# Performance work log

Measured on AMD Instinct MI355X. Metric: run time of the kernel, lower is better.

## Reference

```python
import jax, jax.numpy as jnp
import numpy as np

N, D_IN, D_H, D_OUT, R, E, NB = 50000, 128, 128, 64, 4, 400000, 2

def _xavier(k, shape, fan_in, fan_out):
    # torch xavier_uniform with relu gain sqrt(2)
    lim = np.sqrt(2.0) * np.sqrt(6.0 / (fan_in + fan_out))
    return jax.random.uniform(k, shape, jnp.float32, -lim, lim)

def setup_inputs() -> dict:
    key = jax.random.key(0)
    ks = jax.random.split(key, 9)
    x = jax.random.normal(ks[0], (N, D_IN), dtype=jnp.float32)
    src = jax.random.randint(ks[1], (R, E), 0, N, dtype=jnp.int32)
    dst = jax.random.randint(ks[2], (R, E), 0, N, dtype=jnp.int32)
    inp = {"x": x, "src": src, "dst": dst}
    dims = [(D_IN, D_H), (D_H, D_H), (D_H, D_OUT)]
    for i, (di, do) in enumerate(dims):
        inp[f"basis{i}"] = _xavier(ks[3 + 2 * i], (NB, di, do), di, do)
        inp[f"coeff{i}"] = _xavier(ks[4 + 2 * i], (R, NB), NB, R)
    return inp

def _rel_layer(h, src, dst, basis, coeff):
    """One RelGraphConvLayer: per-relation basis weight + GraphConv(norm='both'),
    summed over relations (HeteroGraphConv aggregate='sum')."""
    n = h.shape[0]
    W = jnp.einsum('rb,bio->rio', coeff, basis)  # [R, d_in, d_out] basis-decomposed weights
    out = jnp.zeros((n, W.shape[-1]), dtype=h.dtype)
    for r in range(src.shape[0]):  # fixed small set of relations
        s, d = src[r], dst[r]
        ones = jnp.ones(s.shape[0], dtype=h.dtype)
        deg_out = jnp.maximum(jax.ops.segment_sum(ones, s, num_segments=n), 1.0)
        deg_in = jnp.maximum(jax.ops.segment_sum(ones, d, num_segments=n), 1.0)
        norm_src = deg_out ** -0.5
        norm_dst = deg_in ** -0.5
        # weight applied before aggregation (d_in >= d_out path of dgl GraphConv; math identical)
        hr = (h * norm_src[:, None]) @ W[r]            # [N, d_out]
        agg = jax.ops.segment_sum(hr[s], d, num_segments=n)  # SpMM via gather + scatter-add
        out = out + agg * norm_dst[:, None]
    return out

def reference(x, src, dst, basis0, coeff0, basis1, coeff1, basis2, coeff2):
    h = jax.nn.relu(_rel_layer(x, src, dst, basis0, coeff0))
    h = jax.nn.relu(_rel_layer(h, src, dst, basis1, coeff1))
    return _rel_layer(h, src, dst, basis2, coeff2)  # final layer: no activation
```

## Files before the change

kernel.cpp:

```cpp
#include <hip/hip_runtime.h>
#include <hip/hip_bf16.h>
#include <cstdint>
#include <cstddef>

#define NN 50000
#define RR 4
#define EE 400000
#define TE (RR*EE)
#define HR 25000
#define RN (RR*NN)
#define NSEG (NN*RR)
#define SCB2 782
#define NBK 512
#define BKSZ 98
#define CHA 4000
#define MAXSPAN 4608

using frag_ab = __attribute__((ext_vector_type(8))) short;
using frag_cd = __attribute__((ext_vector_type(4))) float;

static __device__ __forceinline__ unsigned short f2bf(float f) {
    union { float f; unsigned u; } v; v.f = f;
    unsigned r = (v.u + 0x7FFF + ((v.u >> 16) & 1)) >> 16;
    return (unsigned short)r;
}
static __device__ __forceinline__ unsigned pack2(float lo, float hi) {
    return (unsigned)f2bf(lo) | ((unsigned)f2bf(hi) << 16);
}
static __device__ __forceinline__ float blo(unsigned u) { return __uint_as_float(u << 16); }
static __device__ __forceinline__ float bhi(unsigned u) { return __uint_as_float(u & 0xFFFF0000u); }

__global__ __launch_bounds__(1024) void k_hist(const int* __restrict__ src,
                                               const int* __restrict__ dst,
                                               int* __restrict__ cnt_srcQ,
                                               int* __restrict__ cnt_dstQ) {
    __shared__ unsigned bins[HR / 2];
    int combo = blockIdx.x >> 3;
    int range = (blockIdx.x >> 2) & 1;
    int qc    = blockIdx.x & 3;
    int r = combo >> 1;
    int side = combo & 1;
    const int* arr = (side == 0 ? src : dst) + (size_t)r * EE + (size_t)qc * (EE / 4);
    int lo = range * HR;
    for (int i = threadIdx.x; i < HR / 2; i += 1024) bins[i] = 0;
    __syncthreads();
    const int4* a4 = (const int4*)arr;
    for (int i = threadIdx.x; i < EE / 16; i += 1024) {
        int4 v = a4[i];
        int t;
        t = v.x - lo; if ((unsigned)t < (unsigned)HR) atomicAdd(&bins[t >> 1], 1u << ((t & 1) * 16));
        t = v.y - lo; if ((unsigned)t < (unsigned)HR) atomicAdd(&bins[t >> 1], 1u << ((t & 1) * 16));
        t = v.z - lo; if ((unsigned)t < (unsigned)HR) atomicAdd(&bins[t >> 1], 1u << ((t & 1) * 16));
        t = v.w - lo; if ((unsigned)t < (unsigned)HR) atomicAdd(&bins[t >> 1], 1u << ((t & 1) * 16));
    }
    __syncthreads();
    int* outp = (side == 0 ? cnt_srcQ : cnt_dstQ) + (size_t)qc * RN + (size_t)r * NN + lo;
    for (int i = threadIdx.x; i < HR / 2; i += 1024) {
        unsigned b = bins[i];
        outp[2 * i]     = (int)(b & 0xFFFFu);
        outp[2 * i + 1] = (int)(b >> 16);
    }
}

__global__ __launch_bounds__(256) void k_sum_norms(const int* __restrict__ cnt_srcQ,
                                                   const int* __restrict__ cnt_dstQ,
                                                   float* __restrict__ nsrc,
                                                   float* __restrict__ ndst,
                                                   int* __restrict__ cntd2) {
    int i = blockIdx.x * 256 + threadIdx.x;
    if (i >= RN) return;
    int ss = cnt_srcQ[i] + cnt_srcQ[RN + i] + cnt_srcQ[2 * RN + i] + cnt_srcQ[3 * RN + i];
    int ds = cnt_dstQ[i] + cnt_dstQ[RN + i] + cnt_dstQ[2 * RN + i] + cnt_dstQ[3 * RN + i];
    nsrc[i] = 1.0f / sqrtf(fmaxf((float)ss, 1.0f));
    ndst[i] = 1.0f / sqrtf(fmaxf((float)ds, 1.0f));
    int r = i / NN, d = i - r * NN;
    cntd2[d * 4 + r] = ds;
}

__global__ __launch_bounds__(256) void k_partial(const int* __restrict__ cntd2,
                                                 int* __restrict__ part) {
    __shared__ int s[256];
    int t = threadIdx.x;
    int f = blockIdx.x * 256 + t;
    int v = (f < NSEG) ? cntd2[f] : 0;
    s[t] = v;
    __syncthreads();
    for (int off = 128; off > 0; off >>= 1) {
        if (t < off) s[t] += s[t + off];
        __syncthreads();
    }
    if (t == 0) part[blockIdx.x] = s[0];
}

__global__ __launch_bounds__(1024) void k_scan_small(const int* __restrict__ part,
                                                     int* __restrict__ offs) {
    __shared__ int s[1024];
    int t = threadIdx.x;
    s[t] = (t < SCB2) ? part[t] : 0;
    __syncthreads();
    for (int off = 1; off < 1024; off <<= 1) {
        int v = (t >= off) ? s[t - off] : 0;
        __syncthreads();
        s[t] += v;
        __syncthreads();
    }
    if (t < SCB2) offs[t] = (t == 0) ? 0 : s[t - 1];
}

__global__ __launch_bounds__(256) void k_emit(const int* __restrict__ cntd2,
                                              const int* __restrict__ offs,
                                              int* __restrict__ rp2) {
    __shared__ int s[256];
    int t = threadIdx.x;
    int f = blockIdx.x * 256 + t;
    int v = (f < NSEG) ? cntd2[f] : 0;
    s[t] = v;
    __syncthreads();
    for (int off = 1; off < 256; off <<= 1) {
        int u = (t >= off) ? s[t - off] : 0;
        __syncthreads();
        s[t] += u;
        __syncthreads();
    }
    if (f < NSEG) rp2[f] = offs[blockIdx.x] + s[t] - v;
    if (f == NSEG - 1) rp2[NSEG] = TE;
}

__global__ __launch_bounds__(256) void k_initg(const int* __restrict__ rp2,
                                               int* __restrict__ gcur) {
    int i = blockIdx.x * 256 + threadIdx.x;
    if (i < NBK) gcur[i] = rp2[min(i * BKSZ * 4, NSEG)];
}

__global__ __launch_bounds__(256) void k_fillA(const int* __restrict__ src,
                                               const int* __restrict__ dst,
                                               int* __restrict__ gcur,
                                               unsigned* __restrict__ stage) {
    __shared__ int cnt[NBK];
    __shared__ int rcur[NBK];
    int r = blockIdx.y;
    int base_e = blockIdx.x * CHA;
    int t = threadIdx.x;
    for (int i = t; i < NBK; i += 256) cnt[i] = 0;
    __syncthreads();
    const int* dr = dst + (size_t)r * EE;
    const int* sr = src + (size_t)r * EE;
    for (int i = base_e + t; i < base_e + CHA; i += 256) {
        int d = dr[i];
        atomicAdd(&cnt[d / BKSZ], 1);
    }
    __syncthreads();
    for (int i = t; i < NBK; i += 256) rcur[i] = atomicAdd(&gcur[i], cnt[i]);
    __syncthreads();
    for (int i = base_e + t; i < base_e + CHA; i += 256) {
        int d = dr[i];
        int s = sr[i];
        int b = d / BKSZ;
        int dl = d - b * BKSZ;
        int pos = atomicAdd(&rcur[b], 1);
        stage[pos] = (unsigned)s | ((unsigned)r << 16) | ((unsigned)dl << 18);
    }
}

__global__ __launch_bounds__(256) void k_fillB(const unsigned* __restrict__ stage,
                                               const int* __restrict__ rp2,
                                               const float* __restrict__ nsrc,
                                               const float* __restrict__ ndst,
                                               uint2* __restrict__ ed) {
    __shared__ unsigned imgU[MAXSPAN];
    __shared__ float imgW[MAXSPAN];
    __shared__ int lcur[BKSZ * 4];
    __shared__ float ndL[BKSZ * 4];
    int b = blockIdx.x;
    int t = threadIdx.x;
    int node0 = b * BKSZ;
    if (node0 >= NN) return;
    int nodes = min(BKSZ, NN - node0);
    int nseg_local = nodes * 4;
    int segbase = node0 * 4;
    for (int i = t; i < nseg_local; i += 256) {
        lcur[i] = rp2[segbase + i];
        ndL[i] = ndst[(i & 3) * NN + node0 + (i >> 2)];
    }
    __syncthreads();
    int S0 = rp2[segbase];
    int S1 = rp2[segbase + nseg_local];
    int span = S1 - S0;
    if (span <= MAXSPAN) {
        for (int i = S0 + t; i < S1; i += 256) {
            unsigned w = stage[i];
            int s = (int)(w & 0xFFFFu);
            int r = (int)((w >> 16) & 3u);
            int dl = (int)(w >> 18);
            int seg = dl * 4 + r;
            int pos = atomicAdd(&lcur[seg], 1);
            int idx = pos - S0;
            imgU[idx] = w & 0x3FFFFu;
            imgW[idx] = nsrc[r * NN + s] * ndL[seg];
        }
        __syncthreads();
        for (int i = t; i < span; i += 256)
            ed[S0 + i] = make_uint2(imgU[i], __float_as_uint(imgW[i]));
    } else {
        for (int i = S0 + t; i < S1; i += 256) {
            unsigned w = stage[i];
            int s = (int)(w & 0xFFFFu);
            int r = (int)((w >> 16) & 3u);
            int dl = (int)(w >> 18);
            int seg = dl * 4 + r;
            int pos = atomicAdd(&lcur[seg], 1);
            ed[pos] = make_uint2(w & 0x3FFFFu,
                                 __float_as_uint(nsrc[r * NN + s] * ndL[seg]));
        }
    }
}

__global__ __launch_bounds__(256) void k_cvt_x(const float4* __restrict__ x4,
                                               uint2* __restrict__ o, int n4) {
    int i = blockIdx.x * 256 + threadIdx.x;
    if (i >= n4) return;
    float4 v = x4[i];
    o[i] = make_uint2(pack2(v.x, v.y), pack2(v.z, v.w));
}

__global__ __launch_bounds__(256) void k_cvt_bt_all(const float* __restrict__ B0,
                                                    const float* __restrict__ B1,
                                                    const float* __restrict__ B2,
                                                    unsigned short* __restrict__ Bt0,
                                                    unsigned short* __restrict__ Bt1,
                                                    unsigned short* __restrict__ Bt2) {
    int o = blockIdx.x * 256 + threadIdx.x;
    if (o < 32768) {
        int k = o & 255, n = o >> 8;
        Bt0[o] = f2bf(B0[k * 128 + n]);
    } else if (o < 65536) {
        int i = o - 32768;
        int k = i & 255, n = i >> 8;
        Bt1[i] = f2bf(B1[k * 128 + n]);
    } else if (o < 81920) {
        int i = o - 65536;
        int k = i & 255, n = i >> 8;
        Bt2[i] = f2bf(B2[k * 64 + n]);
    }
}

__global__ __launch_bounds__(256) void k_agg(const uint4* __restrict__ hb4,
                                             const int* __restrict__ rp2,
                                             const uint2* __restrict__ ed,
                                             const float* __restrict__ coeff,
                                             uint2* __restrict__ Mb2) {
    int wave = (blockIdx.x * 256 + threadIdx.x) >> 6;
    int lane = threadIdx.x & 63;
    if (wave >= NN) return;
    int q = lane >> 4, hl = lane & 15;

    float c00 = coeff[0], c01 = coeff[1], c10 = coeff[2], c11 = coeff[3];
    float c20 = coeff[4], c21 = coeff[5], c30 = coeff[6], c31 = coeff[7];

    float a00 = 0.f, a01 = 0.f, a02 = 0.f, a03 = 0.f;
    float a04 = 0.f, a05 = 0.f, a06 = 0.f, a07 = 0.f;
    float a10 = 0.f, a11 = 0.f, a12 = 0.f, a13 = 0.f;
    float a14 = 0.f, a15 = 0.f, a16 = 0.f, a17 = 0.f;

    int e0 = rp2[wave * 4], e1 = rp2[wave * 4 + 4];

    int e = e0;
    uint2 wA = make_uint2(0u, 0u), wB = make_uint2(0u, 0u);
    if (e + 7 < e1) { wA = ed[e + q]; wB = ed[e + 4 + q]; }
    for (; e + 7 < e1; e += 8) {
        uint4 hA = hb4[(size_t)(wA.x & 0xFFFFu) * 16 + hl];
        uint4 hB = hb4[(size_t)(wB.x & 0xFFFFu) * 16 + hl];
        int eN = (e + 15 < e1) ? (e + 8) : e0;
        uint2 nA = ed[eN + q];
        uint2 nB = ed[eN + 4 + q];

        int rA = (int)(wA.x >> 16);
        int rB = (int)(wB.x >> 16);
        float wsA = __uint_as_float(wA.y);
        float wsB = __uint_as_float(wB.y);
        float wa0 = (rA == 0 ? c00 : rA == 1 ? c10 : rA == 2 ? c20 : c30) * wsA;
        float wa1 = (rA == 0 ? c01 : rA == 1 ? c11 : rA == 2 ? c21 : c31) * wsA;
        float wb0 = (rB == 0 ? c00 : rB == 1 ? c10 : rB == 2 ? c20 : c30) * wsB;
        float wb1 = (rB == 0 ? c01 : rB == 1 ? c11 : rB == 2 ? c21 : c31) * wsB;

        float h0 = blo(hA.x), h1 = bhi(hA.x), h2 = blo(hA.y), h3 = bhi(hA.y);
        float h4 = blo(hA.z), h5 = bhi(hA.z), h6 = blo(hA.w), h7 = bhi(hA.w);
        a00 += wa0 * h0; a01 += wa0 * h1; a02 += wa0 * h2; a03 += wa0 * h3;
        a04 += wa0 * h4; a05 += wa0 * h5; a06 += wa0 * h6; a07 += wa0 * h7;
        a10 += wa1 * h0; a11 += wa1 * h1; a12 += wa1 * h2; a13 += wa1 * h3;
        a14 += wa1 * h4; a15 += wa1 * h5; a16 += wa1 * h6; a17 += wa1 * h7;

        h0 = blo(hB.x); h1 = bhi(hB.x); h2 = blo(hB.y); h3 = bhi(hB.y);
        h4 = blo(hB.z); h5 = bhi(hB.z); h6 = blo(hB.w); h7 = bhi(hB.w);
        a00 += wb0 * h0; a01 += wb0 * h1; a02 += wb0 * h2; a03 += wb0 * h3;
        a04 += wb0 * h4; a05 += wb0 * h5; a06 += wb0 * h6; a07 += wb0 * h7;
        a10 += wb1 * h0; a11 += wb1 * h1; a12 += wb1 * h2; a13 += wb1 * h3;
        a14 += wb1 * h4; a15 += wb1 * h5; a16 += wb1 * h6; a17 += wb1 * h7;

        wA = nA; wB = nB;
    }
    for (; e < e1; e += 4) {
        int E = e + q;
        bool act = E < e1;
        uint2 weA = ed[act ? E : e0];
        uint4 hA = hb4[(size_t)(weA.x & 0xFFFFu) * 16 + hl];
        int rA = (int)(weA.x >> 16);
        float wsA = act ? __uint_as_float(weA.y) : 0.f;
        float wa0 = (rA == 0 ? c00 : rA == 1 ? c10 : rA == 2 ? c20 : c30) * wsA;
        float wa1 = (rA == 0 ? c01 : rA == 1 ? c11 : rA == 2 ? c21 : c31) * wsA;
        float h0 = blo(hA.x), h1 = bhi(hA.x), h2 = blo(hA.y), h3 = bhi(hA.y);
        float h4 = blo(hA.z), h5 = bhi(hA.z), h6 = blo(hA.w), h7 = bhi(hA.w);
        a00 += wa0 * h0; a01 += wa0 * h1; a02 += wa0 * h2; a03 += wa0 * h3;
        a04 += wa0 * h4; a05 += wa0 * h5; a06 += wa0 * h6; a07 += wa0 * h7;
        a10 += wa1 * h0; a11 += wa1 * h1; a12 += wa1 * h2; a13 += wa1 * h3;
        a14 += wa1 * h4; a15 += wa1 * h5; a16 += wa1 * h6; a17 += wa1 * h7;
    }

    a00 += __shfl_xor(a00, 16, 64); a00 += __shfl_xor(a00, 32, 64);
    a01 += __shfl_xor(a01, 16, 64); a01 += __shfl_xor(a01, 32, 64);
    a02 += __shfl_xor(a02, 16, 64); a02 += __shfl_xor(a02, 32, 64);
    a03 += __shfl_xor(a03, 16, 64); a03 += __shfl_xor(a03, 32, 64);
    a04 += __shfl_xor(a04, 16, 64); a04 += __shfl_xor(a04, 32, 64);
    a05 += __shfl_xor(a05, 16, 64); a05 += __shfl_xor(a05, 32, 64);
    a06 += __shfl_xor(a06, 16, 64); a06 += __shfl_xor(a06, 32, 64);
    a07 += __shfl_xor(a07, 16, 64); a07 += __shfl_xor(a07, 32, 64);
    a10 += __shfl_xor(a10, 16, 64); a10 += __shfl_xor(a10, 32, 64);
    a11 += __shfl_xor(a11, 16, 64); a11 += __shfl_xor(a11, 32, 64);
    a12 += __shfl_xor(a12, 16, 64); a12 += __shfl_xor(a12, 32, 64);
    a13 += __shfl_xor(a13, 16, 64); a13 += __shfl_xor(a13, 32, 64);
    a14 += __shfl_xor(a14, 16, 64); a14 += __shfl_xor(a14, 32, 64);
    a15 += __shfl_xor(a15, 16, 64); a15 += __shfl_xor(a15, 32, 64);
    a16 += __shfl_xor(a16, 16, 64); a16 += __shfl_xor(a16, 32, 64);
    a17 += __shfl_xor(a17, 16, 64); a17 += __shfl_xor(a17, 32, 64);

    int c = q >> 1, h4 = q & 1;
    float v0 = c ? (h4 ? a14 : a10) : (h4 ? a04 : a00);
    float v1 = c ? (h4 ? a15 : a11) : (h4 ? a05 : a01);
    float v2 = c ? (h4 ? a16 : a12) : (h4 ? a06 : a02);
    float v3 = c ? (h4 ? a17 : a13) : (h4 ? a07 : a03);
    uint2 st;
    st.x = pack2(v0, v1);
    st.y = pack2(v2, v3);
    Mb2[(size_t)wave * 64 + c * 32 + hl * 2 + h4] = st;
}

template <int BN, bool BF16OUT>
__global__ __launch_bounds__(256) void k_gemm(const unsigned short* __restrict__ A,
                                              const unsigned short* __restrict__ Bt,
                                              void* __restrict__ Cout) {
    int wave = threadIdx.x >> 6, lane = threadIdx.x & 63;
    int row0 = blockIdx.x * 64 + wave * 16;
    if (row0 >= NN) return;
    int m = lane & 15, q = lane >> 4;
    const int NT = BN / 16;

    frag_cd acc[NT];
#pragma unroll
    for (int ct = 0; ct < NT; ct++) acc[ct] = (frag_cd){0.f, 0.f, 0.f, 0.f};

    const size_t abase = (size_t)(row0 + m) * 256 + q * 8;
#pragma unroll
    for (int kc = 0; kc < 8; kc++) {
        frag_ab a = *(const frag_ab*)(A + abase + kc * 32);
#pragma unroll
        for (int ct = 0; ct < NT; ct++) {
            frag_ab b = *(const frag_ab*)(Bt + (size_t)(ct * 16 + m) * 256 + kc * 32 + q * 8);
            acc[ct] = __builtin_amdgcn_mfma_f32_16x16x32_bf16(a, b, acc[ct], 0, 0, 0);
        }
    }

#pragma unroll
    for (int ct = 0; ct < NT; ct++) {
#pragma unroll
        for (int i = 0; i < 4; i++) {
            int row = row0 + q * 4 + i;
            int col = ct * 16 + m;
            float v = acc[ct][i];
            if (BF16OUT) {
                v = fmaxf(v, 0.f);
                ((unsigned short*)Cout)[(size_t)row * BN + col] = f2bf(v);
            } else {
                ((float*)Cout)[(size_t)row * BN + col] = v;
            }
        }
    }
}


extern "C" void kernel_launch(void* const* d_in, const int* in_sizes, int n_in,
                              void* d_out, int out_size, void* d_ws, size_t ws_size,
                              hipStream_t stream) {
    const float* x      = (const float*)d_in[0];
    const int*   src    = (const int*)d_in[1];
    const int*   dst    = (const int*)d_in[2];
    const float* basis0 = (const float*)d_in[3];
    const float* coeff0 = (const float*)d_in[4];
    const float* basis1 = (const float*)d_in[5];
    const float* coeff1 = (const float*)d_in[6];
    const float* basis2 = (const float*)d_in[7];
    const float* coeff2 = (const float*)d_in[8];
    float* out = (float*)d_out;

    char* p = (char*)d_ws;
    auto alloc = [&](size_t bytes) {
        char* r = p;
        p += (bytes + 255) & ~(size_t)255;
        return r;
    };
    int*   cnt_srcQ = (int*)alloc((size_t)4 * RN * 4);
    int*   cnt_dstQ = (int*)alloc((size_t)4 * RN * 4);
    float* nsrc     = (float*)alloc((size_t)RN * 4);
    float* ndst     = (float*)alloc((size_t)RN * 4);
    int*   cntd2    = (int*)alloc((size_t)NSEG * 4);
    int*   rp2      = (int*)alloc((size_t)(NSEG + 1) * 4);
    int*   part     = (int*)alloc((size_t)SCB2 * 4);
    int*   offs     = (int*)alloc((size_t)SCB2 * 4);
    int*   gcur     = (int*)alloc((size_t)NBK * 4);
    unsigned* stage = (unsigned*)alloc((size_t)TE * 4);
    uint2* ed       = (uint2*)alloc((size_t)TE * 8);
    unsigned* Mb   = (unsigned*)alloc((size_t)NN * 128 * 4);
    unsigned* Hb   = (unsigned*)alloc((size_t)NN * 64 * 4);
    unsigned* Xb   = (unsigned*)alloc((size_t)NN * 64 * 4);
    unsigned short* Bt0 = (unsigned short*)alloc((size_t)128 * 256 * 2);
    unsigned short* Bt1 = (unsigned short*)alloc((size_t)128 * 256 * 2);
    unsigned short* Bt2 = (unsigned short*)alloc((size_t)64 * 256 * 2);

    k_cvt_x<<<(NN * 32 + 255) / 256, 256, 0, stream>>>((const float4*)x, (uint2*)Xb, NN * 32);
    k_cvt_bt_all<<<320, 256, 0, stream>>>(basis0, basis1, basis2, Bt0, Bt1, Bt2);
    k_hist<<<64, 1024, 0, stream>>>(src, dst, cnt_srcQ, cnt_dstQ);
    k_sum_norms<<<(RN + 255) / 256, 256, 0, stream>>>(cnt_srcQ, cnt_dstQ, nsrc, ndst, cntd2);
    k_partial<<<SCB2, 256, 0, stream>>>(cntd2, part);
    k_scan_small<<<1, 1024, 0, stream>>>(part, offs);
    k_emit<<<SCB2, 256, 0, stream>>>(cntd2, offs, rp2);
    k_initg<<<(NBK + 255) / 256, 256, 0, stream>>>(rp2, gcur);
    k_fillA<<<dim3(EE / CHA, RR), 256, 0, stream>>>(src, dst, gcur, stage);
    k_fillB<<<NBK, 256, 0, stream>>>(stage, rp2, nsrc, ndst, ed);

    int aggBlocks = NN / 4;
    int gemmBlocks = (NN + 63) / 64;

    k_agg<<<aggBlocks, 256, 0, stream>>>((const uint4*)Xb, rp2, ed, coeff0, (uint2*)Mb);
    k_gemm<128, true><<<gemmBlocks, 256, 0, stream>>>((const unsigned short*)Mb, Bt0, Hb);
    k_agg<<<aggBlocks, 256, 0, stream>>>((const uint4*)Hb, rp2, ed, coeff1, (uint2*)Mb);
    k_gemm<128, true><<<gemmBlocks, 256, 0, stream>>>((const unsigned short*)Mb, Bt1, Hb);
    k_agg<<<aggBlocks, 256, 0, stream>>>((const uint4*)Hb, rp2, ed, coeff2, (uint2*)Mb);
    k_gemm<64, false><<<gemmBlocks, 256, 0, stream>>>((const unsigned short*)Mb, Bt2, out);
}
```

Baseline: 407.9 us.

## Assign each quarter-wave one relation segment and factor coefficients out of aggregation

Each 16-lane quarter of the wave now walks the edge segment of a single relation (using per-relation row pointers rp2[wave*4+q]), accumulating 8 plain weighted sums. The basis coefficients are applied once after the loop instead of being selected and multiplied per edge. This cuts the per-edge FMAs in half and removes the relation-select logic. The cost is load imbalance across quarters when relation degrees differ, and a less coalesced edge-index load pattern with shorter unrolled chunks.

Result: slower. 418.2 us (+2.5%).

```diff
diff --git a/kernel.cpp b/kernel.cpp
--- a/kernel.cpp
+++ b/kernel.cpp
@@ -254,67 +254,52 @@
     if (wave >= NN) return;
     int q = lane >> 4, hl = lane & 15;
 
-    float c00 = coeff[0], c01 = coeff[1], c10 = coeff[2], c11 = coeff[3];
-    float c20 = coeff[4], c21 = coeff[5], c30 = coeff[6], c31 = coeff[7];
-
-    float a00 = 0.f, a01 = 0.f, a02 = 0.f, a03 = 0.f;
-    float a04 = 0.f, a05 = 0.f, a06 = 0.f, a07 = 0.f;
-    float a10 = 0.f, a11 = 0.f, a12 = 0.f, a13 = 0.f;
-    float a14 = 0.f, a15 = 0.f, a16 = 0.f, a17 = 0.f;
-
-    int e0 = rp2[wave * 4], e1 = rp2[wave * 4 + 4];
-
-    int e = e0;
+    float cq0 = coeff[2 * q];
+    float cq1 = coeff[2 * q + 1];
+
+    float s0 = 0.f, s1 = 0.f, s2 = 0.f, s3 = 0.f;
+    float s4 = 0.f, s5 = 0.f, s6 = 0.f, s7 = 0.f;
+
+    int e  = rp2[wave * 4 + q];
+    int e1 = rp2[wave * 4 + q + 1];
+
     uint2 wA = make_uint2(0u, 0u), wB = make_uint2(0u, 0u);
-    if (e + 7 < e1) { wA = ed[e + q]; wB = ed[e + 4 + q]; }
-    for (; e + 7 < e1; e += 8) {
+    if (e + 1 < e1) { wA = ed[e]; wB = ed[e + 1]; }
+    for (; e + 1 < e1; e += 2) {
         uint4 hA = hb4[(size_t)(wA.x & 0xFFFFu) * 16 + hl];
         uint4 hB = hb4[(size_t)(wB.x & 0xFFFFu) * 16 + hl];
-        int eN = (e + 15 < e1) ? (e + 8) : e0;
-        uint2 nA = ed[eN + q];
-        uint2 nB = ed[eN + 4 + q];
-
-        int rA = (int)(wA.x >> 16);
-        int rB = (int)(wB.x >> 16);
+        int eN = (e + 3 < e1) ? (e + 2) : e;
+        uint2 nA = ed[eN];
+        uint2 nB = ed[eN + 1];
         float wsA = __uint_as_float(wA.y);
         float wsB = __uint_as_float(wB.y);
-        float wa0 = (rA == 0 ? c00 : rA == 1 ? c10 : rA == 2 ? c20 : c30) * wsA;
-        float wa1 = (rA == 0 ? c01 : rA == 1 ? c11 : rA == 2 ? c21 : c31) * wsA;
-        float wb0 = (rB == 0 ? c00 : rB == 1 ? c10 : rB == 2 ? c20 : c30) * wsB;
-        float wb1 = (rB == 0 ? c01 : rB == 1 ? c11 : rB == 2 ? c21 : c31) * wsB;
-
-        float h0 = blo(hA.x), h1 = bhi(hA.x), h2 = blo(hA.y), h3 = bhi(hA.y);
-        float h4 = blo(hA.z), h5 = bhi(hA.z), h6 = blo(hA.w), h7 = bhi(hA.w);
-        a00 += wa0 * h0; a01 += wa0 * h1; a02 += wa0 * h2; a03 += wa0 * h3;
-        a04 += wa0 * h4; a05 += wa0 * h5; a06 += wa0 * h6; a07 += wa0 * h7;
-        a10 += wa1 * h0; a11 += wa1 * h1; a12 += wa1 * h2; a13 += wa1 * h3;
-        a14 += wa1 * h4; a15 += wa1 * h5; a16 += wa1 * h6; a17 += wa1 * h7;
-
-        h0 = blo(hB.x); h1 = bhi(hB.x); h2 = blo(hB.y); h3 = bhi(hB.y);
-        h4 = blo(hB.z); h5 = bhi(hB.z); h6 = blo(hB.w); h7 = bhi(hB.w);
-        a00 += wb0 * h0; a01 += wb0 * h1; a02 += wb0 * h2; a03 += wb0 * h3;
-        a04 += wb0 * h4; a05 += wb0 * h5; a06 += wb0 * h6; a07 += wb0 * h7;
-        a10 += wb1 * h0; a11 += wb1 * h1; a12 += wb1 * h2; a13 += wb1 * h3;
-        a14 += wb1 * h4; a15 += wb1 * h5; a16 += wb1 * h6; a17 += wb1 * h7;
+
+        s0 += wsA * blo(hA.x); s1 += wsA * bhi(hA.x);
+        s2 += wsA * blo(hA.y); s3 += wsA * bhi(hA.y);
+        s4 += wsA * blo(hA.z); s5 += wsA * bhi(hA.z);
+        s6 += wsA * blo(hA.w); s7 += wsA * bhi(hA.w);
+
+        s0 += wsB * blo(hB.x); s1 += wsB * bhi(hB.x);
+        s2 += wsB * blo(hB.y); s3 += wsB * bhi(hB.y);
+        s4 += wsB * blo(hB.z); s5 += wsB * bhi(hB.z);
+        s6 += wsB * blo(hB.w); s7 += wsB * bhi(hB.w);
 
         wA = nA; wB = nB;
     }
-    for (; e < e1; e += 4) {
-        int E = e + q;
-        bool act = E < e1;
-        uint2 weA = ed[act ? E : e0];
-        uint4 hA = hb4[(size_t)(weA.x & 0xFFFFu) * 16 + hl];
-        int rA = (int)(weA.x >> 16);
-        float wsA = act ? __uint_as_float(weA.y) : 0.f;
-        float wa0 = (rA == 0 ? c00 : rA == 1 ? c10 : rA == 2 ? c20 : c30) * wsA;
-        float wa1 = (rA == 0 ? c01 : rA == 1 ? c11 : rA == 2 ? c21 : c31) * wsA;
-        float h0 = blo(hA.x), h1 = bhi(hA.x), h2 = blo(hA.y), h3 = bhi(hA.y);
-        float h4 = blo(hA.z), h5 = bhi(hA.z), h6 = blo(hA.w), h7 = bhi(hA.w);
-        a00 += wa0 * h0; a01 += wa0 * h1; a02 += wa0 * h2; a03 += wa0 * h3;
-        a04 += wa0 * h4; a05 += wa0 * h5; a06 += wa0 * h6; a07 += wa0 * h7;
-        a10 += wa1 * h0; a11 += wa1 * h1; a12 += wa1 * h2; a13 += wa1 * h3;
-        a14 += wa1 * h4; a15 += wa1 * h5; a16 += wa1 * h6; a17 += wa1 * h7;
-    }
+    if (e < e1) {
+        uint2 w1 = ed[e];
+        uint4 h1 = hb4[(size_t)(w1.x & 0xFFFFu) * 16 + hl];
+        float ws = __uint_as_float(w1.y);
+        s0 += ws * blo(h1.x); s1 += ws * bhi(h1.x);
+        s2 += ws * blo(h1.y); s3 += ws * bhi(h1.y);
+        s4 += ws * blo(h1.z); s5 += ws * bhi(h1.z);
+        s6 += ws * blo(h1.w); s7 += ws * bhi(h1.w);
+    }
+
+    float a00 = cq0 * s0, a01 = cq0 * s1, a02 = cq0 * s2, a03 = cq0 * s3;
+    float a04 = cq0 * s4, a05 = cq0 * s5, a06 = cq0 * s6, a07 = cq0 * s7;
+    float a10 = cq1 * s0, a11 = cq1 * s1, a12 = cq1 * s2, a13 = cq1 * s3;
+    float a14 = cq1 * s4, a15 = cq1 * s5, a16 = cq1 * s6, a17 = cq1 * s7;
 
     a00 += __shfl_xor(a00, 16, 64); a00 += __shfl_xor(a00, 32, 64);
     a01 += __shfl_xor(a01, 16, 64); a01 += __shfl_xor(a01, 32, 64);
```

## Fuse aggregation with basis GEMM per block via swizzled LDS tile

Applied to the files above, without the earlier changes.

Merges each layer's gather-aggregate kernel and the following MFMA GEMM into one kernel. Each 512-thread block aggregates 32 nodes into a swizzled LDS tile, then runs the bf16 MFMA from LDS, so the intermediate Mb matrix no longer goes through global memory. Also merges the x and basis conversion kernels, and folds k_initg into k_emit to cut launches. The cost is lower per-block parallelism in the GEMM phase and a block-wide barrier between the gather and the matmul, plus a ping-pong buffer for layer outputs.

After: 378.3 us. 7.3% less time.

```diff
diff --git a/kernel.cpp b/kernel.cpp
--- a/kernel.cpp
+++ b/kernel.cpp
@@ -109,7 +109,8 @@
 
 __global__ __launch_bounds__(256) void k_emit(const int* __restrict__ cntd2,
                                               const int* __restrict__ offs,
-                                              int* __restrict__ rp2) {
+                                              int* __restrict__ rp2,
+                                              int* __restrict__ gcur) {
     __shared__ int s[256];
     int t = threadIdx.x;
     int f = blockIdx.x * 256 + t;
@@ -122,14 +123,15 @@
         s[t] += u;
         __syncthreads();
     }
-    if (f < NSEG) rp2[f] = offs[blockIdx.x] + s[t] - v;
-    if (f == NSEG - 1) rp2[NSEG] = TE;
-}
-
-__global__ __launch_bounds__(256) void k_initg(const int* __restrict__ rp2,
-                                               int* __restrict__ gcur) {
-    int i = blockIdx.x * 256 + threadIdx.x;
-    if (i < NBK) gcur[i] = rp2[min(i * BKSZ * 4, NSEG)];
+    if (f < NSEG) {
+        int rv = offs[blockIdx.x] + s[t] - v;
+        rp2[f] = rv;
+        if (f % (BKSZ * 4) == 0) gcur[f / (BKSZ * 4)] = rv;
+    }
+    if (f == NSEG - 1) {
+        rp2[NSEG] = TE;
+        gcur[NBK - 1] = TE;
+    }
 }
 
 __global__ __launch_bounds__(256) void k_fillA(const int* __restrict__ src,
@@ -215,172 +217,186 @@
     }
 }
 
-__global__ __launch_bounds__(256) void k_cvt_x(const float4* __restrict__ x4,
-                                               uint2* __restrict__ o, int n4) {
-    int i = blockIdx.x * 256 + threadIdx.x;
-    if (i >= n4) return;
-    float4 v = x4[i];
-    o[i] = make_uint2(pack2(v.x, v.y), pack2(v.z, v.w));
-}
-
-__global__ __launch_bounds__(256) void k_cvt_bt_all(const float* __restrict__ B0,
-                                                    const float* __restrict__ B1,
-                                                    const float* __restrict__ B2,
-                                                    unsigned short* __restrict__ Bt0,
-                                                    unsigned short* __restrict__ Bt1,
-                                                    unsigned short* __restrict__ Bt2) {
-    int o = blockIdx.x * 256 + threadIdx.x;
-    if (o < 32768) {
-        int k = o & 255, n = o >> 8;
-        Bt0[o] = f2bf(B0[k * 128 + n]);
-    } else if (o < 65536) {
-        int i = o - 32768;
-        int k = i & 255, n = i >> 8;
-        Bt1[i] = f2bf(B1[k * 128 + n]);
-    } else if (o < 81920) {
-        int i = o - 65536;
-        int k = i & 255, n = i >> 8;
-        Bt2[i] = f2bf(B2[k * 64 + n]);
-    }
-}
-
-__global__ __launch_bounds__(256) void k_agg(const uint4* __restrict__ hb4,
-                                             const int* __restrict__ rp2,
-                                             const uint2* __restrict__ ed,
-                                             const float* __restrict__ coeff,
-                                             uint2* __restrict__ Mb2) {
-    int wave = (blockIdx.x * 256 + threadIdx.x) >> 6;
+__global__ __launch_bounds__(256) void k_cvt_all(const float4* __restrict__ x4,
+                                                 uint2* __restrict__ o,
+                                                 const float* __restrict__ B0,
+                                                 const float* __restrict__ B1,
+                                                 const float* __restrict__ B2,
+                                                 unsigned short* __restrict__ Bt0,
+                                                 unsigned short* __restrict__ Bt1,
+                                                 unsigned short* __restrict__ Bt2) {
+    int b = blockIdx.x;
+    if (b < 6250) {
+        int i = b * 256 + threadIdx.x;
+        float4 v = x4[i];
+        o[i] = make_uint2(pack2(v.x, v.y), pack2(v.z, v.w));
+    } else {
+        int t = (b - 6250) * 256 + threadIdx.x;
+        if (t < 32768) {
+            int k = t & 255, n = t >> 8;
+            Bt0[t] = f2bf(B0[k * 128 + n]);
+        } else if (t < 65536) {
+            int i = t - 32768;
+            int k = i & 255, n = i >> 8;
+            Bt1[i] = f2bf(B1[k * 128 + n]);
+        } else if (t < 81920) {
+            int i = t - 65536;
+            int k = i & 255, n = i >> 8;
+            Bt2[i] = f2bf(B2[k * 64 + n]);
+        }
+    }
+}
+
+template <int BN, bool BF16OUT>
+__global__ __launch_bounds__(512) void k_agg_gemm(const uint4* __restrict__ hb4,
+                                                  const int* __restrict__ rp2,
+                                                  const uint2* __restrict__ ed,
+                                                  const float* __restrict__ coeff,
+                                                  const unsigned short* __restrict__ Bt,
+                                                  void* __restrict__ Cout) {
+    __shared__ uint4 ldsA4[32 * 32];
+    char* ldsB = (char*)ldsA4;
+
+    int w = threadIdx.x >> 6;
     int lane = threadIdx.x & 63;
-    if (wave >= NN) return;
     int q = lane >> 4, hl = lane & 15;
+    int node0 = blockIdx.x * 32;
 
     float c00 = coeff[0], c01 = coeff[1], c10 = coeff[2], c11 = coeff[3];
     float c20 = coeff[4], c21 = coeff[5], c30 = coeff[6], c31 = coeff[7];
 
-    float a00 = 0.f, a01 = 0.f, a02 = 0.f, a03 = 0.f;
-    float a04 = 0.f, a05 = 0.f, a06 = 0.f, a07 = 0.f;
-    float a10 = 0.f, a11 = 0.f, a12 = 0.f, a13 = 0.f;
-    float a14 = 0.f, a15 = 0.f, a16 = 0.f, a17 = 0.f;
-
-    int e0 = rp2[wave * 4], e1 = rp2[wave * 4 + 4];
-
-    int e = e0;
-    uint2 wA = make_uint2(0u, 0u), wB = make_uint2(0u, 0u);
-    if (e + 7 < e1) { wA = ed[e + q]; wB = ed[e + 4 + q]; }
-    for (; e + 7 < e1; e += 8) {
-        uint4 hA = hb4[(size_t)(wA.x & 0xFFFFu) * 16 + hl];
-        uint4 hB = hb4[(size_t)(wB.x & 0xFFFFu) * 16 + hl];
-        int eN = (e + 15 < e1) ? (e + 8) : e0;
-        uint2 nA = ed[eN + q];
-        uint2 nB = ed[eN + 4 + q];
-
-        int rA = (int)(wA.x >> 16);
-        int rB = (int)(wB.x >> 16);
-        float wsA = __uint_as_float(wA.y);
-        float wsB = __uint_as_float(wB.y);
-        float wa0 = (rA == 0 ? c00 : rA == 1 ? c10 : rA == 2 ? c20 : c30) * wsA;
-        float wa1 = (rA == 0 ? c01 : rA == 1 ? c11 : rA == 2 ? c21 : c31) * wsA;
-        float wb0 = (rB == 0 ? c00 : rB == 1 ? c10 : rB == 2 ? c20 : c30) * wsB;
-        float wb1 = (rB == 0 ? c01 : rB == 1 ? c11 : rB == 2 ? c21 : c31) * wsB;
-
-        float h0 = blo(hA.x), h1 = bhi(hA.x), h2 = blo(hA.y), h3 = bhi(hA.y);
-        float h4 = blo(hA.z), h5 = bhi(hA.z), h6 = blo(hA.w), h7 = bhi(hA.w);
-        a00 += wa0 * h0; a01 += wa0 * h1; a02 += wa0 * h2; a03 += wa0 * h3;
-        a04 += wa0 * h4; a05 += wa0 * h5; a06 += wa0 * h6; a07 += wa0 * h7;
-        a10 += wa1 * h0; a11 += wa1 * h1; a12 += wa1 * h2; a13 += wa1 * h3;
-        a14 += wa1 * h4; a15 += wa1 * h5; a16 += wa1 * h6; a17 += wa1 * h7;
-
-        h0 = blo(hB.x); h1 = bhi(hB.x); h2 = blo(hB.y); h3 = bhi(hB.y);
-        h4 = blo(hB.z); h5 = bhi(hB.z); h6 = blo(hB.w); h7 = bhi(hB.w);
-        a00 += wb0 * h0; a01 += wb0 * h1; a02 += wb0 * h2; a03 += wb0 * h3;
-        a04 += wb0 * h4; a05 += wb0 * h5; a06 += wb0 * h6; a07 += wb0 * h7;
-        a10 += wb1 * h0; a11 += wb1 * h1; a12 += wb1 * h2; a13 += wb1 * h3;
-        a14 += wb1 * h4; a15 += wb1 * h5; a16 += wb1 * h6; a17 += wb1 * h7;
-
-        wA = nA; wB = nB;
-    }
-    for (; e < e1; e += 4) {
-        int E = e + q;
-        bool act = E < e1;
-        uint2 weA = ed[act ? E : e0];
-        uint4 hA = hb4[(size_t)(weA.x & 0xFFFFu) * 16 + hl];
-        int rA = (int)(weA.x >> 16);
-        float wsA = act ? __uint_as_float(weA.y) : 0.f;
-        float wa0 = (rA == 0 ? c00 : rA == 1 ? c10 : rA == 2 ? c20 : c30) * wsA;
-        float wa1 = (rA == 0 ? c01 : rA == 1 ? c11 : rA == 2 ? c21 : c31) * wsA;
-        float h0 = blo(hA.x), h1 = bhi(hA.x), h2 = blo(hA.y), h3 = bhi(hA.y);
-        float h4 = blo(hA.z), h5 = bhi(hA.z), h6 = blo(hA.w), h7 = bhi(hA.w);
-        a00 += wa0 * h0; a01 += wa0 * h1; a02 += wa0 * h2; a03 += wa0 * h3;
-        a04 += wa0 * h4; a05 += wa0 * h5; a06 += wa0 * h6; a07 += wa0 * h7;
-        a10 += wa1 * h0; a11 += wa1 * h1; a12 += wa1 * h2; a13 += wa1 * h3;
-        a14 += wa1 * h4; a15 += wa1 * h5; a16 += wa1 * h6; a17 += wa1 * h7;
-    }
-
-    a00 += __shfl_xor(a00, 16, 64); a00 += __shfl_xor(a00, 32, 64);
-    a01 += __shfl_xor(a01, 16, 64); a01 += __shfl_xor(a01, 32, 64);
-    a02 += __shfl_xor(a02, 16, 64); a02 += __shfl_xor(a02, 32, 64);
-    a03 += __shfl_xor(a03, 16, 64); a03 += __shfl_xor(a03, 32, 64);
-    a04 += __shfl_xor(a04, 16, 64); a04 += __shfl_xor(a04, 32, 64);
-    a05 += __shfl_xor(a05, 16, 64); a05 += __shfl_xor(a05, 32, 64);
-    a06 += __shfl_xor(a06, 16, 64); a06 += __shfl_xor(a06, 32, 64);
-    a07 += __shfl_xor(a07, 16, 64); a07 += __shfl_xor(a07, 32, 64);
-    a10 += __shfl_xor(a10, 16, 64); a10 += __shfl_xor(a10, 32, 64);
-    a11 += __shfl_xor(a11, 16, 64); a11 += __shfl_xor(a11, 32, 64);
-    a12 += __shfl_xor(a12, 16, 64); a12 += __shfl_xor(a12, 32, 64);
-    a13 += __shfl_xor(a13, 16, 64); a13 += __shfl_xor(a13, 32, 64);
-    a14 += __shfl_xor(a14, 16, 64); a14 += __shfl_xor(a14, 32, 64);
-    a15 += __shfl_xor(a15, 16, 64); a15 += __shfl_xor(a15, 32, 64);
-    a16 += __shfl_xor(a16, 16, 64); a16 += __shfl_xor(a16, 32, 64);
-    a17 += __shfl_xor(a17, 16, 64); a17 += __shfl_xor(a17, 32, 64);
-
-    int c = q >> 1, h4 = q & 1;
-    float v0 = c ? (h4 ? a14 : a10) : (h4 ? a04 : a00);
-    float v1 = c ? (h4 ? a15 : a11) : (h4 ? a05 : a01);
-    float v2 = c ? (h4 ? a16 : a12) : (h4 ? a06 : a02);
-    float v3 = c ? (h4 ? a17 : a13) : (h4 ? a07 : a03);
-    uint2 st;
-    st.x = pack2(v0, v1);
-    st.y = pack2(v2, v3);
-    Mb2[(size_t)wave * 64 + c * 32 + hl * 2 + h4] = st;
-}
-
-template <int BN, bool BF16OUT>
-__global__ __launch_bounds__(256) void k_gemm(const unsigned short* __restrict__ A,
-                                              const unsigned short* __restrict__ Bt,
-                                              void* __restrict__ Cout) {
-    int wave = threadIdx.x >> 6, lane = threadIdx.x & 63;
-    int row0 = blockIdx.x * 64 + wave * 16;
-    if (row0 >= NN) return;
-    int m = lane & 15, q = lane >> 4;
-    const int NT = BN / 16;
-
-    frag_cd acc[NT];
+#pragma unroll 1
+    for (int k4 = 0; k4 < 4; k4++) {
+        int rowl = w + k4 * 8;
+        int node = node0 + rowl;
+        if (node < NN) {
+            float a00 = 0.f, a01 = 0.f, a02 = 0.f, a03 = 0.f;
+            float a04 = 0.f, a05 = 0.f, a06 = 0.f, a07 = 0.f;
+            float a10 = 0.f, a11 = 0.f, a12 = 0.f, a13 = 0.f;
+            float a14 = 0.f, a15 = 0.f, a16 = 0.f, a17 = 0.f;
+
+            int e0 = rp2[node * 4], e1 = rp2[node * 4 + 4];
+            int e = e0;
+            uint2 wA = make_uint2(0u, 0u), wB = make_uint2(0u, 0u);
+            if (e + 7 < e1) { wA = ed[e + q]; wB = ed[e + 4 + q]; }
+            for (; e + 7 < e1; e += 8) {
+                uint4 hA = hb4[(size_t)(wA.x & 0xFFFFu) * 16 + hl];
+                uint4 hB = hb4[(size_t)(wB.x & 0xFFFFu) * 16 + hl];
+                int eN = (e + 15 < e1) ? (e + 8) : e0;
+                uint2 nA = ed[eN + q];
+                uint2 nB = ed[eN + 4 + q];
+
+                int rA = (int)(wA.x >> 16);
+                int rB = (int)(wB.x >> 16);
+                float wsA = __uint_as_float(wA.y);
+                float wsB = __uint_as_float(wB.y);
+                float wa0 = (rA == 0 ? c00 : rA == 1 ? c10 : rA == 2 ? c20 : c30) * wsA;
+                float wa1 = (rA == 0 ? c01 : rA == 1 ? c11 : rA == 2 ? c21 : c31) * wsA;
+                float wb0 = (rB == 0 ? c00 : rB == 1 ? c10 : rB == 2 ? c20 : c30) * wsB;
+                float wb1 = (rB == 0 ? c01 : rB == 1 ? c11 : rB == 2 ? c21 : c31) * wsB;
+
+                float h0 = blo(hA.x), h1 = bhi(hA.x), h2 = blo(hA.y), h3 = bhi(hA.y);
+                float h4 = blo(hA.z), h5 = bhi(hA.z), h6 = blo(hA.w), h7 = bhi(hA.w);
+                a00 += wa0 * h0; a01 += wa0 * h1; a02 += wa0 * h2; a03 += wa0 * h3;
+                a04 += wa0 * h4; a05 += wa0 * h5; a06 += wa0 * h6; a07 += wa0 * h7;
+                a10 += wa1 * h0; a11 += wa1 * h1; a12 += wa1 * h2; a13 += wa1 * h3;
+                a14 += wa1 * h4; a15 += wa1 * h5; a16 += wa1 * h6; a17 += wa1 * h7;
+
+                h0 = blo(hB.x); h1 = bhi(hB.x); h2 = blo(hB.y); h3 = bhi(hB.y);
+                h4 = blo(hB.z); h5 = bhi(hB.z); h6 = blo(hB.w); h7 = bhi(hB.w);
+                a00 += wb0 * h0; a01 += wb0 * h1; a02 += wb0 * h2; a03 += wb0 * h3;
+                a04 += wb0 * h4; a05 += wb0 * h5; a06 += wb0 * h6; a07 += wb0 * h7;
+                a10 += wb1 * h0; a11 += wb1 * h1; a12 += wb1 * h2; a13 += wb1 * h3;
+                a14 += wb1 * h4; a15 += wb1 * h5; a16 += wb1 * h6; a17 += wb1 * h7;
+
+                wA = nA; wB = nB;
+            }
+            for (; e < e1; e += 4) {
+                int E = e + q;
+                bool act = E < e1;
+                uint2 weA = ed[act ? E : e0];
+                uint4 hA = hb4[(size_t)(weA.x & 0xFFFFu) * 16 + hl];
+                int rA = (int)(weA.x >> 16);
+                float wsA = act ? __uint_as_float(weA.y) : 0.f;
+                float wa0 = (rA == 0 ? c00 : rA == 1 ? c10 : rA == 2 ? c20 : c30) * wsA;
+                float wa1 = (rA == 0 ? c01 : rA == 1 ? c11 : rA == 2 ? c21 : c31) * wsA;
+                float h0 = blo(hA.x), h1 = bhi(hA.x), h2 = blo(hA.y), h3 = bhi(hA.y);
+                float h4 = blo(hA.z), h5 = bhi(hA.z), h6 = blo(hA.w), h7 = bhi(hA.w);
+                a00 += wa0 * h0; a01 += wa0 * h1; a02 += wa0 * h2; a03 += wa0 * h3;
+                a04 += wa0 * h4; a05 += wa0 * h5; a06 += wa0 * h6; a07 += wa0 * h7;
+                a10 += wa1 * h0; a11 += wa1 * h1; a12 += wa1 * h2; a13 += wa1 * h3;
+                a14 += wa1 * h4; a15 += wa1 * h5; a16 += wa1 * h6; a17 += wa1 * h7;
+            }
+
+            a00 += __shfl_xor(a00, 16, 64); a00 += __shfl_xor(a00, 32, 64);
+            a01 += __shfl_xor(a01, 16, 64); a01 += __shfl_xor(a01, 32, 64);
+            a02 += __shfl_xor(a02, 16, 64); a02 += __shfl_xor(a02, 32, 64);
+            a03 += __shfl_xor(a03, 16, 64); a03 += __shfl_xor(a03, 32, 64);
+            a04 += __shfl_xor(a04, 16, 64); a04 += __shfl_xor(a04, 32, 64);
+            a05 += __shfl_xor(a05, 16, 64); a05 += __shfl_xor(a05, 32, 64);
+            a06 += __shfl_xor(a06, 16, 64); a06 += __shfl_xor(a06, 32, 64);
+            a07 += __shfl_xor(a07, 16, 64); a07 += __shfl_xor(a07, 32, 64);
+            a10 += __shfl_xor(a10, 16, 64); a10 += __shfl_xor(a10, 32, 64);
+            a11 += __shfl_xor(a11, 16, 64); a11 += __shfl_xor(a11, 32, 64);
+            a12 += __shfl_xor(a12, 16, 64); a12 += __shfl_xor(a12, 32, 64);
+            a13 += __shfl_xor(a13, 16, 64); a13 += __shfl_xor(a13, 32, 64);
+            a14 += __shfl_xor(a14, 16, 64); a14 += __shfl_xor(a14, 32, 64);
+            a15 += __shfl_xor(a15, 16, 64); a15 += __shfl_xor(a15, 32, 64);
+            a16 += __shfl_xor(a16, 16, 64); a16 += __shfl_xor(a16, 32, 64);
+            a17 += __shfl_xor(a17, 16, 64); a17 += __shfl_xor(a17, 32, 64);
+
+            int c = q >> 1, h4 = q & 1;
+            float v0 = c ? (h4 ? a14 : a10) : (h4 ? a04 : a00);
+            float v1 = c ? (h4 ? a15 : a11) : (h4 ? a05 : a01);
+            float v2 = c ? (h4 ? a16 : a12) : (h4 ? a06 : a02);
+            float v3 = c ? (h4 ? a17 : a13) : (h4 ? a07 : a03);
+            uint2 st;
+            st.x = pack2(v0, v1);
+            st.y = pack2(v2, v3);
+            int idx8 = c * 32 + hl * 2 + h4;
+            int boff = rowl * 512 + ((idx8 * 8) ^ ((rowl & 7) << 4));
+            *(uint2*)(ldsB + boff) = st;
+        }
+    }
+    __syncthreads();
+
+    int strip = w & 1;
+    int colgrp = w >> 1;
+    int m = lane & 15, qq = lane >> 4;
+    constexpr int NTW = BN / 64;
+
+    frag_cd acc[NTW];
 #pragma unroll
-    for (int ct = 0; ct < NT; ct++) acc[ct] = (frag_cd){0.f, 0.f, 0.f, 0.f};
-
-    const size_t abase = (size_t)(row0 + m) * 256 + q * 8;
+    for (int t = 0; t < NTW; t++) acc[t] = (frag_cd){0.f, 0.f, 0.f, 0.f};
+
+    int arow = strip * 16 + m;
 #pragma unroll
     for (int kc = 0; kc < 8; kc++) {
-        frag_ab a = *(const frag_ab*)(A + abase + kc * 32);
+        int aoff = arow * 512 + ((qq * 16 + kc * 64) ^ ((arow & 7) << 4));
+        frag_ab a = *(const frag_ab*)(ldsB + aoff);
 #pragma unroll
-        for (int ct = 0; ct < NT; ct++) {
-            frag_ab b = *(const frag_ab*)(Bt + (size_t)(ct * 16 + m) * 256 + kc * 32 + q * 8);
-            acc[ct] = __builtin_amdgcn_mfma_f32_16x16x32_bf16(a, b, acc[ct], 0, 0, 0);
-        }
-    }
-
+        for (int t = 0; t < NTW; t++) {
+            int ct = colgrp * NTW + t;
+            frag_ab b = *(const frag_ab*)(Bt + (size_t)(ct * 16 + m) * 256 + kc * 32 + qq * 8);
+            acc[t] = __builtin_amdgcn_mfma_f32_16x16x32_bf16(a, b, acc[t], 0, 0, 0);
+        }
+    }
+
+    int row0 = node0 + strip * 16;
 #pragma unroll
-    for (int ct = 0; ct < NT; ct++) {
+    for (int t = 0; t < NTW; t++) {
 #pragma unroll
         for (int i = 0; i < 4; i++) {
-            int row = row0 + q * 4 + i;
-            int col = ct * 16 + m;
-            float v = acc[ct][i];
-            if (BF16OUT) {
-                v = fmaxf(v, 0.f);
-                ((unsigned short*)Cout)[(size_t)row * BN + col] = f2bf(v);
-            } else {
-                ((float*)Cout)[(size_t)row * BN + col] = v;
+            int row = row0 + qq * 4 + i;
+            if (row < NN) {
+                int col = (colgrp * NTW + t) * 16 + m;
+                float v = acc[t][i];
+                if (BF16OUT) {
+                    v = fmaxf(v, 0.f);
+                    ((unsigned short*)Cout)[(size_t)row * BN + col] = f2bf(v);
+                } else {
+                    ((float*)Cout)[(size_t)row * BN + col] = v;
+                }
             }
         }
     }
@@ -418,31 +434,29 @@
     int*   gcur     = (int*)alloc((size_t)NBK * 4);
     unsigned* stage = (unsigned*)alloc((size_t)TE * 4);
     uint2* ed       = (uint2*)alloc((size_t)TE * 8);
-    unsigned* Mb   = (unsigned*)alloc((size_t)NN * 128 * 4);
-    unsigned* Hb   = (unsigned*)alloc((size_t)NN * 64 * 4);
-    unsigned* Xb   = (unsigned*)alloc((size_t)NN * 64 * 4);
+    unsigned* Hb    = (unsigned*)alloc((size_t)NN * 64 * 4);
+    unsigned* Hb2   = (unsigned*)alloc((size_t)NN * 64 * 4);
+    unsigned* Xb    = (unsigned*)alloc((size_t)NN * 64 * 4);
     unsigned short* Bt0 = (unsigned short*)alloc((size_t)128 * 256 * 2);
     unsigned short* Bt1 = (unsigned short*)alloc((size_t)128 * 256 * 2);
     unsigned short* Bt2 = (unsigned short*)alloc((size_t)64 * 256 * 2);
 
-    k_cvt_x<<<(NN * 32 + 255) / 256, 256, 0, stream>>>((const float4*)x, (uint2*)Xb, NN * 32);
-    k_cvt_bt_all<<<320, 256, 0, stream>>>(basis0, basis1, basis2, Bt0, Bt1, Bt2);
+    k_cvt_all<<<6570, 256, 0, stream>>>((const float4*)x, (uint2*)Xb,
+                                        basis0, basis1, basis2, Bt0, Bt1, Bt2);
     k_hist<<<64, 1024, 0, stream>>>(src, dst, cnt_srcQ, cnt_dstQ);
     k_sum_norms<<<(RN + 255) / 256, 256, 0, stream>>>(cnt_srcQ, cnt_dstQ, nsrc, ndst, cntd2);
     k_partial<<<SCB2, 256, 0, stream>>>(cntd2, part);
     k_scan_small<<<1, 1024, 0, stream>>>(part, offs);
-    k_emit<<<SCB2, 256, 0, stream>>>(cntd2, offs, rp2);
-    k_initg<<<(NBK + 255) / 256, 256, 0, stream>>>(rp2, gcur);
+    k_emit<<<SCB2, 256, 0, stream>>>(cntd2, offs, rp2, gcur);
     k_fillA<<<dim3(EE / CHA, RR), 256, 0, stream>>>(src, dst, gcur, stage);
     k_fillB<<<NBK, 256, 0, stream>>>(stage, rp2, nsrc, ndst, ed);
 
-    int aggBlocks = NN / 4;
-    int gemmBlocks = (NN + 63) / 64;
-
-    k_agg<<<aggBlocks, 256, 0, stream>>>((const uint4*)Xb, rp2, ed, coeff0, (uint2*)Mb);
-    k_gemm<128, true><<<gemmBlocks, 256, 0, stream>>>((const unsigned short*)Mb, Bt0, Hb);
-    k_agg<<<aggBlocks, 256, 0, stream>>>((const uint4*)Hb, rp2, ed, coeff1, (uint2*)Mb);
-    k_gemm<128, true><<<gemmBlocks, 256, 0, stream>>>((const unsigned short*)Mb, Bt1, Hb);
-    k_agg<<<aggBlocks, 256, 0, stream>>>((const uint4*)Hb, rp2, ed, coeff2, (uint2*)Mb);
-    k_gemm<64, false><<<gemmBlocks, 256, 0, stream>>>((const unsigned short*)Mb, Bt2, out);
-}
+    int fusedBlocks = (NN + 31) / 32;
+
+    k_agg_gemm<128, true><<<fusedBlocks, 512, 0, stream>>>(
+        (const uint4*)Xb, rp2, ed, coeff0, Bt0, Hb);
+    k_agg_gemm<128, true><<<fusedBlocks, 512, 0, stream>>>(
+        (const uint4*)Hb, rp2, ed, coeff1, Bt1, Hb2);
+    k_agg_gemm<64, false><<<fusedBlocks, 512, 0, stream>>>(
+        (const uint4*)Hb2, rp2, ed, coeff2, Bt2, out);
+}
```
